# Kernel tuning notes

Hardware: AMD Instinct MI355X
Metric: run time of the kernel (lower is better)

## Reference

```python
import jax, jax.numpy as jnp
import numpy as np

B, L, E, H = 4, 4096, 1024, 16
D = E // H
SQRT_D = float(np.sqrt(D))


def _g(x):
    # torch: softplus(x, beta=5) ** 2
    sp = jax.nn.softplus(5.0 * x) / 5.0
    return sp * sp


def setup_inputs() -> dict:
    key = jax.random.key(0)
    ks = jax.random.split(key, 7)
    s = 1.0 / np.sqrt(E)
    x = jax.random.normal(ks[0], (B, L, E), jnp.float32)
    Wq = jax.random.normal(ks[1], (E, E), jnp.float32) * s
    bq = jax.random.normal(ks[2], (E,), jnp.float32) * s
    Wk = jax.random.normal(ks[3], (E, E), jnp.float32) * s
    bk = jax.random.normal(ks[4], (E,), jnp.float32) * s
    Wv = jax.random.normal(ks[5], (E, E), jnp.float32) * s
    bv = jax.random.normal(ks[6], (E,), jnp.float32) * s
    return {"x": x, "Wq": Wq, "bq": bq, "Wk": Wk, "bk": bk, "Wv": Wv, "bv": bv}


def _fast_linear_attn(q, k, v):
    # q,k,v: [B,S,H,D]
    Ls = q.shape[1]
    # RALA-style global-query rescaling of K
    q_global = q.mean(axis=1, keepdims=True) / SQRT_D          # [B,1,H,D]
    logits = jnp.einsum('bihd,blhd->bihl', q_global, k)        # [B,1,H,L]
    alpha = jax.nn.softmax(logits, axis=-1) * Ls               # [B,1,H,L]
    alpha = jnp.transpose(alpha[:, 0], (0, 2, 1))[..., None]   # [B,L,H,1]
    k = k * alpha
    gq, gk = _g(q), _g(k)
    gmq, gmk = _g(-q), _g(-k)
    # symmetric / antisymmetric KV accumulation: state [B,H,D,D]
    gk_v = jnp.einsum('bshd,bshv->bhdv', gk, v)
    gmk_v = jnp.einsum('bshd,bshv->bhdv', gmk, v)
    num = (jnp.einsum('bshd,bhdv->bshv', gq, gk_v)
           + jnp.einsum('bshd,bhdv->bshv', gmq, gmk_v))        # [B,S,H,D]
    den = (jnp.einsum('bshd,bhd->bsh', gq, gk.sum(axis=1))
           + jnp.einsum('bshd,bhd->bsh', gmq, gmk.sum(axis=1)))
    return num / (den[..., None] + 1e-6)


def reference(x, Wq, bq, Wk, bk, Wv, bv):
    q = (x @ Wq + bq).reshape(B, L, H, D)
    k = (x @ Wk + bk).reshape(B, L, H, D)
    v = (x @ Wv + bv).reshape(B, L, H, D)
    out = _fast_linear_attn(q, k, v)  # [B,L,H,D]
    return out.reshape(B, L, E)
```

## Files before the change

kernel.cpp:

```cpp
#include <hip/hip_runtime.h>
#include <hip/hip_bf16.h>
#include <math.h>

#define B_ 4
#define L_ 4096
#define E_ 1024
#define H_ 16
#define D_ 64
#define M_ (B_*L_)

typedef __attribute__((ext_vector_type(8))) short s8;
typedef __attribute__((ext_vector_type(4))) float f4;

__device__ __forceinline__ float gfun(float x) {
  float z = fminf(5.0f * x, 60.0f);
  float sp = 0.2f * __logf(1.0f + __expf(z));
  return sp * sp;
}

__device__ __forceinline__ unsigned short f2bf(float v) {
  __hip_bfloat16 h = __float2bfloat16(v);
  return *reinterpret_cast<unsigned short*>(&h);
}
__device__ __forceinline__ float bf2f(unsigned short u) {
  __hip_bfloat16 h = *reinterpret_cast<__hip_bfloat16*>(&u);
  return __bfloat162float(h);
}

__device__ __forceinline__ void gload16(const void* g, void* l) {
  __builtin_amdgcn_global_load_lds(
      (const __attribute__((address_space(1))) void*)g,
      (__attribute__((address_space(3))) void*)l, 16, 0, 0);
}

__global__ __launch_bounds__(256) void split_x(
    const float* __restrict__ x, unsigned short* __restrict__ Ah,
    float* __restrict__ xsum)
{
  int blk = blockIdx.x, t = threadIdx.x;
  int r0 = blk * 64, b = r0 >> 12;
  int c4 = t * 4;
  float4 cs = {0.f, 0.f, 0.f, 0.f};
  for (int r = 0; r < 64; ++r) {
    int row = r0 + r;
    float4 x4 = *(const float4*)(x + (size_t)row * E_ + c4);
    ushort4 hi, lo;
    unsigned short h;
    h = f2bf(x4.x); hi.x = h; lo.x = f2bf(x4.x - bf2f(h));
    h = f2bf(x4.y); hi.y = h; lo.y = f2bf(x4.y - bf2f(h));
    h = f2bf(x4.z); hi.z = h; lo.z = f2bf(x4.z - bf2f(h));
    h = f2bf(x4.w); hi.w = h; lo.w = f2bf(x4.w - bf2f(h));
    *(ushort4*)&Ah[(size_t)row * 2048 + c4]        = hi;
    *(ushort4*)&Ah[(size_t)row * 2048 + 1024 + c4] = lo;
    cs.x += x4.x; cs.y += x4.y; cs.z += x4.z; cs.w += x4.w;
  }
  atomicAdd(&xsum[b * E_ + c4 + 0], cs.x);
  atomicAdd(&xsum[b * E_ + c4 + 1], cs.y);
  atomicAdd(&xsum[b * E_ + c4 + 2], cs.z);
  atomicAdd(&xsum[b * E_ + c4 + 3], cs.w);
}

__global__ __launch_bounds__(256) void split_wT(
    const float* __restrict__ Wq, const float* __restrict__ Wk,
    const float* __restrict__ Wv, const float* __restrict__ bq,
    const float* __restrict__ xsum,
    unsigned short* __restrict__ Bt, float* __restrict__ qg)
{
  int z = blockIdx.z;
  const float* W = (z == 0) ? Wq : (z == 1) ? Wk : Wv;
  __shared__ float tile[32][33];
  int t = threadIdx.x;
  int tx = t & 31, ty = t >> 5;
  int k0 = blockIdx.x * 32, n0 = blockIdx.y * 32;
  #pragma unroll
  for (int i = 0; i < 4; ++i)
    tile[ty + i*8][tx] = W[(size_t)(k0 + ty + i*8) * 1024 + n0 + tx];
  __syncthreads();
  unsigned short* Bz = Bt + (size_t)z * 2097152;
  #pragma unroll
  for (int i = 0; i < 4; ++i) {
    int n = n0 + ty + i*8, kk = k0 + tx;
    float v = tile[tx][ty + i*8];
    unsigned short h = f2bf(v);
    Bz[(size_t)n * 2048 + kk]        = h;
    Bz[(size_t)n * 2048 + 1024 + kk] = f2bf(v - bf2f(h));
  }
  if (z == 0 && t < 128) {
    int n = t & 31, b = t >> 5;
    float dot = 0.f;
    #pragma unroll
    for (int kk = 0; kk < 32; ++kk)
      dot += xsum[b * E_ + k0 + kk] * tile[kk][n];
    float val = dot * (1.0f / (L_ * 8.0f));
    if (k0 == 0) val += bq[n0 + n] * 0.125f;
    atomicAdd(&qg[b * E_ + n0 + n], val);
  }
}

#define PRIO1() __builtin_amdgcn_s_setprio(1)
#define PRIO0() __builtin_amdgcn_s_setprio(0)
#define BARR() do { asm volatile("" ::: "memory"); \
                    __builtin_amdgcn_s_barrier(); \
                    asm volatile("" ::: "memory"); } while (0)
#define WAITL0() asm volatile("s_waitcnt lgkmcnt(0)" ::: "memory")
#define WAITV(n) asm volatile("s_waitcnt vmcnt(" n ")" ::: "memory")

#define STAGE_A(buf, kofs) do { \
  const unsigned short* g_ = gA + (kofs); \
  char* d_ = dA0 + (buf) * 32768; \
  gload16(g_,          d_); \
  gload16(g_ + 131072, d_ +  8192); \
  gload16(g_ + 262144, d_ + 16384); \
  gload16(g_ + 393216, d_ + 24576); \
} while (0)

#define STAGE_B(buf, kofs) do { \
  const unsigned short* g_ = gB + (kofs); \
  char* d_ = dB0 + (buf) * 32768; \
  gload16(g_,          d_); \
  gload16(g_ + 131072, d_ +  8192); \
  gload16(g_ + 262144, d_ + 16384); \
  gload16(g_ + 393216, d_ + 24576); \
} while (0)

#define LDA(buf, mh) do { \
  const char* p_ = shb + (buf) * 32768 + arow + (mh) * 8192; \
  _Pragma("unroll") \
  for (int ii = 0; ii < 4; ++ii) { \
    aF[ii][0] = *(const s8*)(p_ + ii * 2048 + c0); \
    aF[ii][1] = *(const s8*)(p_ + ii * 2048 + c1); \
  } \
} while (0)

#define LDB(buf, nh) do { \
  const char* p_ = shb + 65536 + (buf) * 32768 + brow + (nh) * 4096; \
  _Pragma("unroll") \
  for (int jj = 0; jj < 2; ++jj) { \
    bF[(nh)*2+jj][0] = *(const s8*)(p_ + jj * 2048 + c0); \
    bF[(nh)*2+jj][1] = *(const s8*)(p_ + jj * 2048 + c1); \
  } \
} while (0)

#define MFMAQ(mh, nh) do { \
  _Pragma("unroll") \
  for (int ii = 0; ii < 4; ++ii) \
    _Pragma("unroll") \
    for (int jj = 0; jj < 2; ++jj) { \
      acc[(mh)*4+ii][(nh)*2+jj] = __builtin_amdgcn_mfma_f32_16x16x32_bf16( \
          aF[ii][0], bF[(nh)*2+jj][0], acc[(mh)*4+ii][(nh)*2+jj], 0, 0, 0); \
      acc[(mh)*4+ii][(nh)*2+jj] = __builtin_amdgcn_mfma_f32_16x16x32_bf16( \
          aF[ii][1], bF[(nh)*2+jj][1], acc[(mh)*4+ii][(nh)*2+jj], 0, 0, 0); \
    } \
} while (0)

#define TILE4(buf, doStage, kB_, kA_, vmN) do { \
   \
  LDA(buf, 0); LDB(buf, 0); LDB(buf, 1); \
  BARR(); WAITL0(); \
  PRIO1(); MFMAQ(0, 0); PRIO0(); \
  BARR(); \
   \
  if (doStage) STAGE_B(buf, kB_); \
  BARR(); \
  PRIO1(); MFMAQ(0, 1); PRIO0(); \
  BARR(); \
   \
  LDA(buf, 1); \
  BARR(); WAITL0(); \
  PRIO1(); MFMAQ(1, 0); PRIO0(); \
  BARR(); \
   \
  if (doStage) STAGE_A(buf, kA_); \
  BARR(); \
  PRIO1(); MFMAQ(1, 1); PRIO0(); \
  WAITV(vmN); \
  BARR(); \
} while (0)

__global__ __launch_bounds__(512, 2) void qkv_mfma(
    const unsigned short* __restrict__ Ah, const unsigned short* __restrict__ Bt,
    const float* __restrict__ bq, const float* __restrict__ bk,
    const float* __restrict__ bv, const float* __restrict__ qg,
    float* __restrict__ aexp, float* __restrict__ denom,
    float* __restrict__ qo, float* __restrict__ ko, float* __restrict__ vo)
{
  __shared__ unsigned short sh[65536];

  const int t  = threadIdx.x;
  const int li = blockIdx.x;
  const int xc = li & 7;
  const int idx = li >> 3;
  const int z   = idx >> 5;
  const int rem = idx & 31;
  const int bm = (xc * 8 + (rem >> 2)) * 256;
  const int bn = (rem & 3) * 256;

  const float* bias = (z == 0) ? bq : (z == 1) ? bk : bv;
  float* out = (z == 0) ? qo : (z == 1) ? ko : vo;
  const unsigned short* Bz = Bt + (size_t)z * 2097152;

  const int srow = t >> 3;
  const int scol = ((t & 7) ^ (srow & 7)) * 8;
  const unsigned short* gA = Ah + (size_t)(bm + srow) * 2048 + scol;
  const unsigned short* gB = Bz + (size_t)(bn + srow) * 2048 + scol;
  char* const shb = (char*)sh;
  char* const dA0 = shb +         t * 16;
  char* const dB0 = shb + 65536 + t * 16;

  const int lane = t & 63, wid = t >> 6;
  const int wm = wid >> 2, wn = wid & 3;
  const int fr = lane & 15, fq = lane >> 4;
  const int c0 = ((fq)     ^ (fr & 7)) * 16;
  const int c1 = ((fq + 4) ^ (fr & 7)) * 16;
  const int arow = (wm * 128 + fr) * 128;
  const int brow = (wn *  64 + fr) * 128;

  f4 acc[8][4] = {};
  s8 aF[4][2], bF[4][2];

  STAGE_B(0, 0);  STAGE_A(0, 0);
  STAGE_B(1, 64); STAGE_A(1, 64);
  WAITV("8");
  BARR();

  #pragma unroll 1
  for (int it = 0; it < 23; ++it) {
    const int t2 = 2 * it + 2, t3 = 2 * it + 3;
    const int kA2 = (t2 < 16) ? t2 * 64 : t2 * 64 - 1024;
    const int kB2 = (t2 < 32) ? t2 * 64 : t2 * 64 - 2048;
    const int kA3 = (t3 < 16) ? t3 * 64 : t3 * 64 - 1024;
    const int kB3 = (t3 < 32) ? t3 * 64 : t3 * 64 - 2048;
    TILE4(0, true, kB2, kA2, "8");
    TILE4(1, true, kB3, kA3, "8");
  }
  TILE4(0, false, 0, 0, "0");
  TILE4(1, false, 0, 0, "0");

  float bv4[4];
  #pragma unroll
  for (int j = 0; j < 4; ++j) bv4[j] = bias[bn + wn * 64 + j * 16 + fr];
  #pragma unroll
  for (int i = 0; i < 8; ++i) {
    const int mrow = bm + wm * 128 + i * 16 + fq * 4;
    #pragma unroll
    for (int j = 0; j < 4; ++j) {
      const int ncol = bn + wn * 64 + j * 16 + fr;
      #pragma unroll
      for (int r = 0; r < 4; ++r)
        out[(size_t)(mrow + r) * E_ + ncol] = acc[i][j][r] + bv4[j];
    }
  }

  if (z == 1) {
    const int b_ = bm >> 12;
    const int h  = (bn >> 6) + wn;
    const int bh = b_ * 16 + h;
    float qgv[4];
    #pragma unroll
    for (int j = 0; j < 4; ++j) qgv[j] = qg[bh * 64 + j * 16 + fr];
    float partial[8][4];
    #pragma unroll
    for (int i = 0; i < 8; ++i)
      #pragma unroll
      for (int r = 0; r < 4; ++r) {
        float p = 0.f;
        #pragma unroll
        for (int j = 0; j < 4; ++j)
          p += qgv[j] * (acc[i][j][r] + bv4[j]);
        p += __shfl_xor(p, 1);
        p += __shfl_xor(p, 2);
        p += __shfl_xor(p, 4);
        p += __shfl_xor(p, 8);
        partial[i][r] = p;
      }
    if (fr == 0) {
      const int lbase = (bm & 4095) + wm * 128 + fq * 4;
      float s = 0.f;
      #pragma unroll
      for (int i = 0; i < 8; ++i)
        #pragma unroll
        for (int r = 0; r < 4; ++r) {
          float e = __expf(partial[i][r]);
          aexp[(size_t)bh * 4096 + lbase + i * 16 + r] = e;
          s += e;
        }
      atomicAdd(&denom[bh], s);
    }
  }
}

__global__ __launch_bounds__(256) void state_part(
    const float* __restrict__ k, const float* __restrict__ v,
    const float* __restrict__ aexp, const float* __restrict__ denom,
    float* __restrict__ Spart, float* __restrict__ SMpart,
    float* __restrict__ kpart, float* __restrict__ kmpart)
{
  __shared__ unsigned short lds[49152];
  const int bh = blockIdx.x, b = bh >> 4, h = bh & 15;
  const int c = blockIdx.y;
  const int l0 = c * 128;
  const float scale = (float)L_ / denom[bh];
  const int t = threadIdx.x;

  {
    const int lp = t >> 2, c4 = t & 3;
    const size_t r0 = (size_t)(b * L_ + l0 + 2 * lp) * E_ + h * 64;
    float4 k0[4], k1[4], v0[4], v1[4];
    #pragma unroll
    for (int i = 0; i < 4; ++i) {
      const int col = c4 * 4 + i * 16;
      k0[i] = *(const float4*)(k + r0 + col);
      k1[i] = *(const float4*)(k + r0 + E_ + col);
      v0[i] = *(const float4*)(v + r0 + col);
      v1[i] = *(const float4*)(v + r0 + E_ + col);
    }
    const float av0 = aexp[(size_t)bh * L_ + l0 + 2 * lp]     * scale;
    const float av1 = aexp[(size_t)bh * L_ + l0 + 2 * lp + 1] * scale;
    const int usl = 2 * lp;
    #pragma unroll
    for (int i = 0; i < 4; ++i) {
      const float ke[4] = {k0[i].x, k0[i].y, k0[i].z, k0[i].w};
      const float ko[4] = {k1[i].x, k1[i].y, k1[i].z, k1[i].w};
      const float ve[4] = {v0[i].x, v0[i].y, v0[i].z, v0[i].w};
      const float vo[4] = {v1[i].x, v1[i].y, v1[i].z, v1[i].w};
      #pragma unroll
      for (int j = 0; j < 4; ++j) {
        const int d  = c4 * 4 + i * 16 + j;
        const int rb = d * 256, x7 = d & 7;
        const int ph = rb + (((usl      ) >> 3) ^ x7) * 8 + (usl & 7);
        const int pl = rb + (((usl + 128) >> 3) ^ x7) * 8 + (usl & 7);
        const float ge = gfun( ke[j] * av0), go = gfun( ko[j] * av1);
        const float me = gfun(-ke[j] * av0), mo = gfun(-ko[j] * av1);
        unsigned short eh, oh;
        unsigned int w;
        eh = f2bf(ge); oh = f2bf(go);
        w = (unsigned)eh | ((unsigned)oh << 16);
        *(unsigned int*)&lds[ph] = w;
        eh = f2bf(ge - bf2f(eh)); oh = f2bf(go - bf2f(oh));
        w = (unsigned)eh | ((unsigned)oh << 16);
        *(unsigned int*)&lds[pl] = w;
        eh = f2bf(me); oh = f2bf(mo);
        w = (unsigned)eh | ((unsigned)oh << 16);
        *(unsigned int*)&lds[16384 + ph] = w;
        eh = f2bf(me - bf2f(eh)); oh = f2bf(mo - bf2f(oh));
        w = (unsigned)eh | ((unsigned)oh << 16);
        *(unsigned int*)&lds[16384 + pl] = w;
        eh = f2bf(ve[j]); oh = f2bf(vo[j]);
        w = (unsigned)eh | ((unsigned)oh << 16);
        *(unsigned int*)&lds[32768 + ph] = w;
        eh = f2bf(ve[j] - bf2f(eh)); oh = f2bf(vo[j] - bf2f(oh));
        w = (unsigned)eh | ((unsigned)oh << 16);
        *(unsigned int*)&lds[32768 + pl] = w;
      }
    }
  }
  __syncthreads();

  {
    const int wid = t >> 6, lane = t & 63;
    const int s = wid >> 1, dh = wid & 1;
    const int fr = lane & 15, fq = lane >> 4;
    const unsigned short* AT = lds + s * 16384;
    const unsigned short* VT = lds + 32768;
    f4 acc[2][4] = {};
    #pragma unroll
    for (int ks = 0; ks < 12; ++ks) {
      const int seg = ks >> 2, loc = ks & 3;
      const int ac = loc * 32 + fq * 8 + ((seg == 2) ? 128 : 0);
      const int bc = loc * 32 + fq * 8 + ((seg == 1) ? 128 : 0);
      s8 aF[2], bF[4];
      #pragma unroll
      for (int m = 0; m < 2; ++m) {
        const int row = dh * 32 + m * 16 + fr;
        aF[m] = *(const s8*)&AT[row * 256 + ((ac >> 3) ^ (row & 7)) * 8 + (ac & 7)];
      }
      #pragma unroll
      for (int n = 0; n < 4; ++n) {
        const int row = n * 16 + fr;
        bF[n] = *(const s8*)&VT[row * 256 + ((bc >> 3) ^ (row & 7)) * 8 + (bc & 7)];
      }
      #pragma unroll
      for (int m = 0; m < 2; ++m)
        #pragma unroll
        for (int n = 0; n < 4; ++n)
          acc[m][n] = __builtin_amdgcn_mfma_f32_16x16x32_bf16(
              aF[m], bF[n], acc[m][n], 0, 0, 0);
    }
    float* Sp = (s == 0) ? Spart : SMpart;
    const size_t pb = ((size_t)(c * 64 + bh)) * 4096;
    #pragma unroll
    for (int m = 0; m < 2; ++m)
      #pragma unroll
      for (int n = 0; n < 4; ++n)
        #pragma unroll
        for (int r = 0; r < 4; ++r) {
          const int d  = dh * 32 + m * 16 + fq * 4 + r;
          const int vv = n * 16 + fr;
          Sp[pb + d * 64 + vv] = acc[m][n][r];
        }
  }

  if (t < 128) {
    const int isM = t >> 6, d = t & 63;
    const unsigned short* R = lds + isM * 16384 + d * 256;
    const int x7 = d & 7;
    float sum = 0.f;
    #pragma unroll
    for (int sl = 0; sl < 32; ++sl) {
      s8 w8 = *(const s8*)&R[(sl ^ x7) * 8];
      #pragma unroll
      for (int e = 0; e < 8; ++e)
        sum += bf2f((unsigned short)w8[e]);
    }
    (isM ? kmpart : kpart)[(c * 64 + bh) * 64 + d] = sum;
  }
}

__global__ __launch_bounds__(256) void state_reduce(
    const float* __restrict__ Spart, const float* __restrict__ SMpart,
    const float* __restrict__ kpart, const float* __restrict__ kmpart,
    float* __restrict__ S, float* __restrict__ Sm,
    float* __restrict__ ksum, float* __restrict__ kmsum)
{
  int bh = blockIdx.x, seg = blockIdx.y, t = threadIdx.x;
  int idx = seg * 1024 + t * 4;
  float4 s = {0,0,0,0}, sm = {0,0,0,0};
  #pragma unroll
  for (int p = 0; p < 32; ++p) {
    float4 a = *(const float4*)&Spart [((size_t)(p*64 + bh))*4096 + idx];
    float4 c = *(const float4*)&SMpart[((size_t)(p*64 + bh))*4096 + idx];
    s.x += a.x; s.y += a.y; s.z += a.z; s.w += a.w;
    sm.x += c.x; sm.y += c.y; sm.z += c.z; sm.w += c.w;
  }
  *(float4*)&S [(size_t)bh*4096 + idx] = s;
  *(float4*)&Sm[(size_t)bh*4096 + idx] = sm;
  if (seg == 0 && t < 64) {
    float a = 0.f, c = 0.f;
    #pragma unroll
    for (int p = 0; p < 32; ++p) {
      a += kpart [(p*64 + bh)*64 + t];
      c += kmpart[(p*64 + bh)*64 + t];
    }
    ksum [bh*64 + t] = a;
    kmsum[bh*64 + t] = c;
  }
}

__global__ __launch_bounds__(128, 4) void out_kernel(
    const float* __restrict__ q,
    const float* __restrict__ S, const float* __restrict__ Sm,
    const float* __restrict__ ksum, const float* __restrict__ kmsum,
    float* __restrict__ out)
{
  int bh = blockIdx.x; int b = bh >> 4, h = bh & 15;
  int l0 = blockIdx.y * 64;
  __shared__ float Gq[64][64], Gm[64][64];
  int t = threadIdx.x;

  int lr = t >> 1, dq = (t & 1) * 32;
  const float4* qp = (const float4*)(q + (size_t)(b*L_ + l0 + lr)*E_ + h*64 + dq);
  #pragma unroll
  for (int j = 0; j < 8; ++j) {
    float4 qv = qp[j];
    float vals[4] = {qv.x, qv.y, qv.z, qv.w};
    #pragma unroll
    for (int jj = 0; jj < 4; ++jj) {
      int dd = dq + j*4 + jj;
      Gq[dd][lr] = gfun(vals[jj]);
      Gm[dd][lr] = gfun(-vals[jj]);
    }
  }
  __syncthreads();

  int tn = (t & 7) * 8, tm = (t >> 3) * 4;
  const float* Sp   = S  + (size_t)bh*4096;
  const float* Smp  = Sm + (size_t)bh*4096;
  const float* ksp  = ksum  + bh*64;
  const float* kmsp = kmsum + bh*64;
  float acc[4][8] = {};
  float den[4] = {};
  #pragma unroll 2
  for (int kk = 0; kk < 64; ++kk) {
    float4 ga = *(const float4*)&Gq[kk][tm];
    float4 ma = *(const float4*)&Gm[kk][tm];
    float4 s0 = *(const float4*)&Sp [kk*64 + tn];
    float4 s1 = *(const float4*)&Sp [kk*64 + tn + 4];
    float4 m0 = *(const float4*)&Smp[kk*64 + tn];
    float4 m1 = *(const float4*)&Smp[kk*64 + tn + 4];
    float ksv = ksp[kk], kmv = kmsp[kk];
    float gv[4] = {ga.x, ga.y, ga.z, ga.w};
    float mv[4] = {ma.x, ma.y, ma.z, ma.w};
    float sv[8] = {s0.x, s0.y, s0.z, s0.w, s1.x, s1.y, s1.z, s1.w};
    float smv[8] = {m0.x, m0.y, m0.z, m0.w, m1.x, m1.y, m1.z, m1.w};
    #pragma unroll
    for (int i = 0; i < 4; ++i) {
      #pragma unroll
      for (int j = 0; j < 8; ++j)
        acc[i][j] += gv[i]*sv[j] + mv[i]*smv[j];
      den[i] += gv[i]*ksv + mv[i]*kmv;
    }
  }

  #pragma unroll
  for (int i = 0; i < 4; ++i) {
    float r = 1.0f / (den[i] + 1e-6f);
    float4 o0, o1;
    o0.x = acc[i][0]*r; o0.y = acc[i][1]*r; o0.z = acc[i][2]*r; o0.w = acc[i][3]*r;
    o1.x = acc[i][4]*r; o1.y = acc[i][5]*r; o1.z = acc[i][6]*r; o1.w = acc[i][7]*r;
    size_t ro = (size_t)(b*L_ + l0 + tm + i)*E_ + h*64 + tn;
    *(float4*)(out + ro)     = o0;
    *(float4*)(out + ro + 4) = o1;
  }
}

extern "C" void kernel_launch(void* const* d_in, const int* in_sizes, int n_in,
                              void* d_out, int out_size, void* d_ws, size_t ws_size,
                              hipStream_t stream) {
  const float* x  = (const float*)d_in[0];
  const float* Wq = (const float*)d_in[1];
  const float* bq = (const float*)d_in[2];
  const float* Wk = (const float*)d_in[3];
  const float* bk = (const float*)d_in[4];
  const float* Wv = (const float*)d_in[5];
  const float* bv = (const float*)d_in[6];
  float* out = (float*)d_out;
  float* ws  = (float*)d_ws;

  float* q      = ws;
  float* k      = ws + 16777216;
  float* qg     = ws + 33554432;
  float* denom  = ws + 33558528;
  float* xsum   = ws + 33558592;
  float* S      = ws + 33562688;
  float* Sm     = ws + 33824832;
  float* ksum   = ws + 34086976;
  float* kmsum  = ws + 34091072;
  float* aexp   = ws + 34095168;
  unsigned short* Ah = (unsigned short*)(ws + 34357312);
  unsigned short* Bt = (unsigned short*)(ws + 51134528);
  float* Spart  = ws + 34357312;
  float* SMpart = ws + 42745920;
  float* kpart  = ws + 51134528;
  float* kmpart = ws + 51265600;
  float* v      = out;

  hipMemsetAsync(qg, 0, 8256 * sizeof(float), stream);

  split_x<<<256, 256, 0, stream>>>(x, Ah, xsum);
  split_wT<<<dim3(32, 32, 3), 256, 0, stream>>>(Wq, Wk, Wv, bq, xsum, Bt, qg);
  qkv_mfma<<<dim3(768), 512, 0, stream>>>(Ah, Bt, bq, bk, bv, qg,
                                          aexp, denom, q, k, v);
  state_part<<<dim3(B_*H_, 32), 256, 0, stream>>>(k, v, aexp, denom,
                                                  Spart, SMpart, kpart, kmpart);
  state_reduce<<<dim3(B_*H_, 4), 256, 0, stream>>>(Spart, SMpart, kpart, kmpart,
                                                   S, Sm, ksum, kmsum);
  out_kernel<<<dim3(B_*H_, 64), 128, 0, stream>>>(q, S, Sm, ksum, kmsum, out);
}
```

Baseline: 676.5 us.

## Merge GEMM tile phases with fewer barriers; chunk state kernel into two sub-passes

The QKV GEMM inner tile now runs two MFMA quarters back-to-back per LDS read, with fewer workgroup barriers, and issues both global staging loads together. The aim is to cut synchronisation overhead and give each wave longer MFMA runs. The state_part kernel now processes its 128-row chunk as two 64-row sub-passes, which halves its LDS footprint and may raise occupancy. The cost is an extra barrier per sub-pass, and the reordered staging could hurt overlap of global loads with compute.

Measured after the change: 620.4 us. 1.09x faster.

```diff
diff --git a/kernel.cpp b/kernel.cpp
--- a/kernel.cpp
+++ b/kernel.cpp
@@ -153,26 +153,17 @@
     } \
 } while (0)
 
-#define TILE4(buf, doStage, kB_, kA_, vmN) do { \
+#define TILE2(buf, doStage, kB_, kA_, vmN) do { \
    \
   LDA(buf, 0); LDB(buf, 0); LDB(buf, 1); \
-  BARR(); WAITL0(); \
-  PRIO1(); MFMAQ(0, 0); PRIO0(); \
-  BARR(); \
-   \
-  if (doStage) STAGE_B(buf, kB_); \
-  BARR(); \
-  PRIO1(); MFMAQ(0, 1); PRIO0(); \
-  BARR(); \
+  WAITL0(); \
+  PRIO1(); MFMAQ(0, 0); MFMAQ(0, 1); PRIO0(); \
    \
   LDA(buf, 1); \
-  BARR(); WAITL0(); \
-  PRIO1(); MFMAQ(1, 0); PRIO0(); \
   BARR(); \
-   \
-  if (doStage) STAGE_A(buf, kA_); \
-  BARR(); \
-  PRIO1(); MFMAQ(1, 1); PRIO0(); \
+  WAITL0(); \
+  if (doStage) { STAGE_B(buf, kB_); STAGE_A(buf, kA_); } \
+  PRIO1(); MFMAQ(1, 0); MFMAQ(1, 1); PRIO0(); \
   WAITV(vmN); \
   BARR(); \
 } while (0)
@@ -230,11 +221,11 @@
     const int kB2 = (t2 < 32) ? t2 * 64 : t2 * 64 - 2048;
     const int kA3 = (t3 < 16) ? t3 * 64 : t3 * 64 - 1024;
     const int kB3 = (t3 < 32) ? t3 * 64 : t3 * 64 - 2048;
-    TILE4(0, true, kB2, kA2, "8");
-    TILE4(1, true, kB3, kA3, "8");
-  }
-  TILE4(0, false, 0, 0, "0");
-  TILE4(1, false, 0, 0, "0");
+    TILE2(0, true, kB2, kA2, "8");
+    TILE2(1, true, kB3, kA3, "8");
+  }
+  TILE2(0, false, 0, 0, "0");
+  TILE2(1, false, 0, 0, "0");
 
   float bv4[4];
   #pragma unroll
@@ -295,89 +286,81 @@
     float* __restrict__ Spart, float* __restrict__ SMpart,
     float* __restrict__ kpart, float* __restrict__ kmpart)
 {
-  __shared__ unsigned short lds[49152];
+  __shared__ unsigned short lds[24576];
   const int bh = blockIdx.x, b = bh >> 4, h = bh & 15;
   const int c = blockIdx.y;
-  const int l0 = c * 128;
   const float scale = (float)L_ / denom[bh];
   const int t = threadIdx.x;
 
-  {
-    const int lp = t >> 2, c4 = t & 3;
-    const size_t r0 = (size_t)(b * L_ + l0 + 2 * lp) * E_ + h * 64;
-    float4 k0[4], k1[4], v0[4], v1[4];
-    #pragma unroll
-    for (int i = 0; i < 4; ++i) {
-      const int col = c4 * 4 + i * 16;
-      k0[i] = *(const float4*)(k + r0 + col);
-      k1[i] = *(const float4*)(k + r0 + E_ + col);
-      v0[i] = *(const float4*)(v + r0 + col);
-      v1[i] = *(const float4*)(v + r0 + E_ + col);
-    }
-    const float av0 = aexp[(size_t)bh * L_ + l0 + 2 * lp]     * scale;
-    const float av1 = aexp[(size_t)bh * L_ + l0 + 2 * lp + 1] * scale;
+  const int wid = t >> 6, lane = t & 63;
+  const int s = wid >> 1, dh = wid & 1;
+  const int fr = lane & 15, fq = lane >> 4;
+  const int lp = t >> 3, dg8 = (t & 7) * 8;
+  const int kd = t & 63, isM = (t >> 6) & 1;
+  const int kx7 = kd & 7;
+  const unsigned short* AT = lds + s * 8192;
+  const unsigned short* VT = lds + 16384;
+
+  f4 acc[2][4] = {};
+  float ksr = 0.f;
+
+  #pragma unroll 1
+  for (int sc = 0; sc < 2; ++sc) {
+    const int l0 = c * 128 + sc * 64 + 2 * lp;
+    const size_t r0 = (size_t)(b * L_ + l0) * E_ + h * 64 + dg8;
+    float4 kE0 = *(const float4*)(k + r0);
+    float4 kE1 = *(const float4*)(k + r0 + 4);
+    float4 kO0 = *(const float4*)(k + r0 + E_);
+    float4 kO1 = *(const float4*)(k + r0 + E_ + 4);
+    float4 vE0 = *(const float4*)(v + r0);
+    float4 vE1 = *(const float4*)(v + r0 + 4);
+    float4 vO0 = *(const float4*)(v + r0 + E_);
+    float4 vO1 = *(const float4*)(v + r0 + E_ + 4);
+    const float av0 = aexp[(size_t)bh * L_ + l0]     * scale;
+    const float av1 = aexp[(size_t)bh * L_ + l0 + 1] * scale;
+    const float ke[8] = {kE0.x,kE0.y,kE0.z,kE0.w,kE1.x,kE1.y,kE1.z,kE1.w};
+    const float ko[8] = {kO0.x,kO0.y,kO0.z,kO0.w,kO1.x,kO1.y,kO1.z,kO1.w};
+    const float ve[8] = {vE0.x,vE0.y,vE0.z,vE0.w,vE1.x,vE1.y,vE1.z,vE1.w};
+    const float vo[8] = {vO0.x,vO0.y,vO0.z,vO0.w,vO1.x,vO1.y,vO1.z,vO1.w};
+    if (sc) __syncthreads();
     const int usl = 2 * lp;
     #pragma unroll
-    for (int i = 0; i < 4; ++i) {
-      const float ke[4] = {k0[i].x, k0[i].y, k0[i].z, k0[i].w};
-      const float ko[4] = {k1[i].x, k1[i].y, k1[i].z, k1[i].w};
-      const float ve[4] = {v0[i].x, v0[i].y, v0[i].z, v0[i].w};
-      const float vo[4] = {v1[i].x, v1[i].y, v1[i].z, v1[i].w};
-      #pragma unroll
-      for (int j = 0; j < 4; ++j) {
-        const int d  = c4 * 4 + i * 16 + j;
-        const int rb = d * 256, x7 = d & 7;
-        const int ph = rb + (((usl      ) >> 3) ^ x7) * 8 + (usl & 7);
-        const int pl = rb + (((usl + 128) >> 3) ^ x7) * 8 + (usl & 7);
-        const float ge = gfun( ke[j] * av0), go = gfun( ko[j] * av1);
-        const float me = gfun(-ke[j] * av0), mo = gfun(-ko[j] * av1);
-        unsigned short eh, oh;
-        unsigned int w;
-        eh = f2bf(ge); oh = f2bf(go);
-        w = (unsigned)eh | ((unsigned)oh << 16);
-        *(unsigned int*)&lds[ph] = w;
-        eh = f2bf(ge - bf2f(eh)); oh = f2bf(go - bf2f(oh));
-        w = (unsigned)eh | ((unsigned)oh << 16);
-        *(unsigned int*)&lds[pl] = w;
-        eh = f2bf(me); oh = f2bf(mo);
-        w = (unsigned)eh | ((unsigned)oh << 16);
-        *(unsigned int*)&lds[16384 + ph] = w;
-        eh = f2bf(me - bf2f(eh)); oh = f2bf(mo - bf2f(oh));
-        w = (unsigned)eh | ((unsigned)oh << 16);
-        *(unsigned int*)&lds[16384 + pl] = w;
-        eh = f2bf(ve[j]); oh = f2bf(vo[j]);
-        w = (unsigned)eh | ((unsigned)oh << 16);
-        *(unsigned int*)&lds[32768 + ph] = w;
-        eh = f2bf(ve[j] - bf2f(eh)); oh = f2bf(vo[j] - bf2f(oh));
-        w = (unsigned)eh | ((unsigned)oh << 16);
-        *(unsigned int*)&lds[32768 + pl] = w;
-      }
-    }
-  }
-  __syncthreads();
-
-  {
-    const int wid = t >> 6, lane = t & 63;
-    const int s = wid >> 1, dh = wid & 1;
-    const int fr = lane & 15, fq = lane >> 4;
-    const unsigned short* AT = lds + s * 16384;
-    const unsigned short* VT = lds + 32768;
-    f4 acc[2][4] = {};
-    #pragma unroll
-    for (int ks = 0; ks < 12; ++ks) {
-      const int seg = ks >> 2, loc = ks & 3;
-      const int ac = loc * 32 + fq * 8 + ((seg == 2) ? 128 : 0);
-      const int bc = loc * 32 + fq * 8 + ((seg == 1) ? 128 : 0);
+    for (int j = 0; j < 8; ++j) {
+      const int d = dg8 + j, x7 = d & 7;
+      const int ph = d * 128 + (((usl >> 3)) ^ x7) * 8 + (usl & 7);
+      const int pl = ph + 64;
+      const float ge = gfun( ke[j] * av0), go = gfun( ko[j] * av1);
+      const float me = gfun(-ke[j] * av0), mo = gfun(-ko[j] * av1);
+      unsigned short eh, oh;
+      eh = f2bf(ge); oh = f2bf(go);
+      *(unsigned int*)&lds[ph] = (unsigned)eh | ((unsigned)oh << 16);
+      eh = f2bf(ge - bf2f(eh)); oh = f2bf(go - bf2f(oh));
+      *(unsigned int*)&lds[pl] = (unsigned)eh | ((unsigned)oh << 16);
+      eh = f2bf(me); oh = f2bf(mo);
+      *(unsigned int*)&lds[8192 + ph] = (unsigned)eh | ((unsigned)oh << 16);
+      eh = f2bf(me - bf2f(eh)); oh = f2bf(mo - bf2f(oh));
+      *(unsigned int*)&lds[8192 + pl] = (unsigned)eh | ((unsigned)oh << 16);
+      eh = f2bf(ve[j]); oh = f2bf(vo[j]);
+      *(unsigned int*)&lds[16384 + ph] = (unsigned)eh | ((unsigned)oh << 16);
+      eh = f2bf(ve[j] - bf2f(eh)); oh = f2bf(vo[j] - bf2f(oh));
+      *(unsigned int*)&lds[16384 + pl] = (unsigned)eh | ((unsigned)oh << 16);
+    }
+    __syncthreads();
+    #pragma unroll
+    for (int ks = 0; ks < 6; ++ks) {
+      const int seg = ks >> 1, loc = ks & 1;
+      const int ac = loc * 32 + fq * 8 + ((seg == 2) ? 64 : 0);
+      const int bc = loc * 32 + fq * 8 + ((seg == 1) ? 64 : 0);
       s8 aF[2], bF[4];
       #pragma unroll
       for (int m = 0; m < 2; ++m) {
         const int row = dh * 32 + m * 16 + fr;
-        aF[m] = *(const s8*)&AT[row * 256 + ((ac >> 3) ^ (row & 7)) * 8 + (ac & 7)];
+        aF[m] = *(const s8*)&AT[row * 128 + ((ac >> 3) ^ (row & 7)) * 8];
       }
       #pragma unroll
       for (int n = 0; n < 4; ++n) {
         const int row = n * 16 + fr;
-        bF[n] = *(const s8*)&VT[row * 256 + ((bc >> 3) ^ (row & 7)) * 8 + (bc & 7)];
+        bF[n] = *(const s8*)&VT[row * 128 + ((bc >> 3) ^ (row & 7)) * 8];
       }
       #pragma unroll
       for (int m = 0; m < 2; ++m)
@@ -386,34 +369,32 @@
           acc[m][n] = __builtin_amdgcn_mfma_f32_16x16x32_bf16(
               aF[m], bF[n], acc[m][n], 0, 0, 0);
     }
-    float* Sp = (s == 0) ? Spart : SMpart;
-    const size_t pb = ((size_t)(c * 64 + bh)) * 4096;
-    #pragma unroll
-    for (int m = 0; m < 2; ++m)
-      #pragma unroll
-      for (int n = 0; n < 4; ++n)
+    if (t < 128) {
+      const unsigned short* R = lds + isM * 8192 + kd * 128;
+      #pragma unroll
+      for (int sl = 0; sl < 16; ++sl) {
+        s8 w8 = *(const s8*)&R[(sl ^ kx7) * 8];
         #pragma unroll
-        for (int r = 0; r < 4; ++r) {
-          const int d  = dh * 32 + m * 16 + fq * 4 + r;
-          const int vv = n * 16 + fr;
-          Sp[pb + d * 64 + vv] = acc[m][n][r];
-        }
-  }
-
-  if (t < 128) {
-    const int isM = t >> 6, d = t & 63;
-    const unsigned short* R = lds + isM * 16384 + d * 256;
-    const int x7 = d & 7;
-    float sum = 0.f;
-    #pragma unroll
-    for (int sl = 0; sl < 32; ++sl) {
-      s8 w8 = *(const s8*)&R[(sl ^ x7) * 8];
-      #pragma unroll
-      for (int e = 0; e < 8; ++e)
-        sum += bf2f((unsigned short)w8[e]);
-    }
-    (isM ? kmpart : kpart)[(c * 64 + bh) * 64 + d] = sum;
-  }
+        for (int e = 0; e < 8; ++e)
+          ksr += bf2f((unsigned short)w8[e]);
+      }
+    }
+  }
+
+  float* Sp = (s == 0) ? Spart : SMpart;
+  const size_t pb = ((size_t)(c * 64 + bh)) * 4096;
+  #pragma unroll
+  for (int m = 0; m < 2; ++m)
+    #pragma unroll
+    for (int n = 0; n < 4; ++n)
+      #pragma unroll
+      for (int r = 0; r < 4; ++r) {
+        const int d  = dh * 32 + m * 16 + fq * 4 + r;
+        const int vv = n * 16 + fr;
+        Sp[pb + d * 64 + vv] = acc[m][n][r];
+      }
+  if (t < 128)
+    (isM ? kmpart : kpart)[(c * 64 + bh) * 64 + kd] = ksr;
 }
 
 __global__ __launch_bounds__(256) void state_reduce(
```
